# Kernel optimization log

Hardware: AMD Instinct MI355X
Metric: run time of the kernel (lower is better)

Reference implementation:

```python
import jax, jax.numpy as jnp
import numpy as np

BLOCK = 128  # fp8 block-quant block size (128, 128)


def dequant_block_fp8_weight(w, scale_inv):
    """w: [O, I] fp8-valued weights (stored as f32); scale_inv: [O//128, I//128].
    Dequant = per-(128,128)-block multiply by scale."""
    O, I = w.shape
    wb = w.reshape(O // BLOCK, BLOCK, I // BLOCK, BLOCK)
    wb = wb * scale_inv[:, None, :, None]
    return wb.reshape(O, I)


def setup_inputs() -> dict:
    key = jax.random.key(0)
    ks = jax.random.split(key, 7)
    H, F, T = 5120, 1536, 8192  # hidden, moe_intermediate, tokens
    x = jax.random.normal(ks[0], (T, H), dtype=jnp.float32)
    w_gate = jax.random.normal(ks[1], (F, H), dtype=jnp.float32)
    s_gate = jax.random.uniform(ks[2], (F // BLOCK, H // BLOCK), dtype=jnp.float32) * 0.01 + 1e-4
    w_up = jax.random.normal(ks[3], (F, H), dtype=jnp.float32)
    s_up = jax.random.uniform(ks[4], (F // BLOCK, H // BLOCK), dtype=jnp.float32) * 0.01 + 1e-4
    w_down = jax.random.normal(ks[5], (H, F), dtype=jnp.float32)
    s_down = jax.random.uniform(ks[6], (H // BLOCK, F // BLOCK), dtype=jnp.float32) * 0.01 + 1e-4
    return {"x": x, "w_gate": w_gate, "s_gate": s_gate, "w_up": w_up,
            "s_up": s_up, "w_down": w_down, "s_down": s_down}


def reference(x, w_gate, s_gate, w_up, s_up, w_down, s_down):
    # down_proj(silu(gate_proj(x)) * up_proj(x)), each Linear dequantizing
    # block-scaled fp8 weights first (bias=False everywhere).
    wg = dequant_block_fp8_weight(w_gate, s_gate).astype(x.dtype)
    wu = dequant_block_fp8_weight(w_up, s_up).astype(x.dtype)
    wd = dequant_block_fp8_weight(w_down, s_down).astype(x.dtype)
    gate = jnp.einsum('th,fh->tf', x, wg)  # [T, F]
    up = jnp.einsum('th,fh->tf', x, wu)    # [T, F]
    h = jax.nn.silu(gate) * up
    out = jnp.einsum('tf,hf->th', h, wd)   # [T, H]
    return out
```

## Files before the change

kernel.cpp:

```cpp
#include <hip/hip_runtime.h>


typedef __bf16 bf16x8 __attribute__((ext_vector_type(8)));
typedef float  f32x4  __attribute__((ext_vector_type(4)));

#define BK 32

__device__ __forceinline__ void stage128x32(const __bf16* __restrict__ gbase,
                                            __bf16* lds, int ldk, int tid) {
#pragma unroll
  for (int i = 0; i < 2; ++i) {
    int c = tid + i * 256;
    int row = c >> 2;
    int q = c & 3;
    const __bf16* g = gbase + (size_t)row * ldk + q * 8;
    __builtin_amdgcn_global_load_lds(
        (const __attribute__((address_space(1))) void*)g,
        (__attribute__((address_space(3))) void*)(lds + c * 8),
        16, 0, 0);
  }
}

__global__ void xcast(const float* __restrict__ in, __bf16* __restrict__ out,
                      size_t n) {
  size_t idx = ((size_t)blockIdx.x * blockDim.x + threadIdx.x) * 8;
  if (idx >= n) return;
  f32x4 a = *(const f32x4*)(in + idx);
  f32x4 b = *(const f32x4*)(in + idx + 4);
  bf16x8 o;
#pragma unroll
  for (int i = 0; i < 4; ++i) { o[i] = (__bf16)a[i]; o[i + 4] = (__bf16)b[i]; }
  *(bf16x8*)(out + idx) = o;
}

__global__ void dequant8(const float* __restrict__ w,
                         const float* __restrict__ s,
                         __bf16* __restrict__ o, int rows, int cols) {
  size_t idx = ((size_t)blockIdx.x * blockDim.x + threadIdx.x) * 8;
  if (idx >= (size_t)rows * (size_t)cols) return;
  int r = (int)(idx / cols);
  int c = (int)(idx % cols);
  float sc = s[(r >> 7) * (cols >> 7) + (c >> 7)];
  f32x4 a = *(const f32x4*)(w + idx);
  f32x4 b = *(const f32x4*)(w + idx + 4);
  bf16x8 ov;
#pragma unroll
  for (int i = 0; i < 4; ++i) {
    ov[i] = (__bf16)(a[i] * sc);
    ov[i + 4] = (__bf16)(b[i] * sc);
  }
  *(bf16x8*)(o + idx) = ov;
}

__global__ __launch_bounds__(256, 2)
void gateup_gemm(const __bf16* __restrict__ X, const __bf16* __restrict__ Wg,
                 const __bf16* __restrict__ Wu, __bf16* __restrict__ Hout,
                 int M, int N, int K) {
  __shared__ __bf16 sA[128 * BK];
  __shared__ __bf16 sBg[128 * BK];
  __shared__ __bf16 sBu[128 * BK];
  const int tid = threadIdx.x;
  const int lane = tid & 63;
  const int wave = tid >> 6;
  const int wm = (wave >> 1) * 64;
  const int wn = (wave & 1) * 64;
  const int m0 = blockIdx.y * 128;
  const int n0 = blockIdx.x * 128;
  const int lr = lane & 15;
  const int lk = (lane >> 4) * 8;

  f32x4 accg[4][4] = {};
  f32x4 accu[4][4] = {};

  const __bf16* Ab = X + (size_t)m0 * K;
  const __bf16* Gb = Wg + (size_t)n0 * K;
  const __bf16* Ub = Wu + (size_t)n0 * K;

  for (int k0 = 0; k0 < K; k0 += BK) {
    stage128x32(Ab + k0, sA, K, tid);
    stage128x32(Gb + k0, sBg, K, tid);
    stage128x32(Ub + k0, sBu, K, tid);
    __syncthreads();
    bf16x8 af[4];
#pragma unroll
    for (int i = 0; i < 4; ++i)
      af[i] = *(const bf16x8*)(sA + (wm + i * 16 + lr) * BK + lk);
#pragma unroll
    for (int j = 0; j < 4; ++j) {
      bf16x8 bg = *(const bf16x8*)(sBg + (wn + j * 16 + lr) * BK + lk);
      bf16x8 bu = *(const bf16x8*)(sBu + (wn + j * 16 + lr) * BK + lk);
#pragma unroll
      for (int i = 0; i < 4; ++i) {
        accg[i][j] =
            __builtin_amdgcn_mfma_f32_16x16x32_bf16(af[i], bg, accg[i][j], 0, 0, 0);
        accu[i][j] =
            __builtin_amdgcn_mfma_f32_16x16x32_bf16(af[i], bu, accu[i][j], 0, 0, 0);
      }
    }
    __syncthreads();
  }

  const int colb = n0 + wn + lr;
  const int rowb = m0 + wm + (lane >> 4) * 4;
#pragma unroll
  for (int i = 0; i < 4; ++i)
#pragma unroll
    for (int j = 0; j < 4; ++j)
#pragma unroll
      for (int r = 0; r < 4; ++r) {
        float g = accg[i][j][r];
        float u = accu[i][j][r];
        float hv = (g / (1.0f + __expf(-g))) * u;
        Hout[(size_t)(rowb + i * 16 + r) * N + (colb + j * 16)] = (__bf16)hv;
      }
}

__global__ void down_gemm(const __bf16* __restrict__ A,
                          const __bf16* __restrict__ B,
                          float* __restrict__ C, int M, int N, int K) {
  __shared__ __bf16 sA[128 * BK];
  __shared__ __bf16 sB[128 * BK];
  const int tid = threadIdx.x;
  const int lane = tid & 63;
  const int wave = tid >> 6;
  const int wm = (wave >> 1) * 64;
  const int wn = (wave & 1) * 64;
  const int m0 = blockIdx.y * 128;
  const int n0 = blockIdx.x * 128;
  const int lr = lane & 15;
  const int lk = (lane >> 4) * 8;

  f32x4 acc[4][4] = {};

  const __bf16* Ab = A + (size_t)m0 * K;
  const __bf16* Bb = B + (size_t)n0 * K;

  for (int k0 = 0; k0 < K; k0 += BK) {
    stage128x32(Ab + k0, sA, K, tid);
    stage128x32(Bb + k0, sB, K, tid);
    __syncthreads();
    bf16x8 af[4];
#pragma unroll
    for (int i = 0; i < 4; ++i)
      af[i] = *(const bf16x8*)(sA + (wm + i * 16 + lr) * BK + lk);
#pragma unroll
    for (int j = 0; j < 4; ++j) {
      bf16x8 bf = *(const bf16x8*)(sB + (wn + j * 16 + lr) * BK + lk);
#pragma unroll
      for (int i = 0; i < 4; ++i)
        acc[i][j] =
            __builtin_amdgcn_mfma_f32_16x16x32_bf16(af[i], bf, acc[i][j], 0, 0, 0);
    }
    __syncthreads();
  }

  const int colb = n0 + wn + lr;
  const int rowb = m0 + wm + (lane >> 4) * 4;
#pragma unroll
  for (int i = 0; i < 4; ++i)
#pragma unroll
    for (int j = 0; j < 4; ++j)
#pragma unroll
      for (int r = 0; r < 4; ++r)
        C[(size_t)(rowb + i * 16 + r) * N + (colb + j * 16)] = acc[i][j][r];
}

extern "C" void kernel_launch(void* const* d_in, const int* in_sizes, int n_in,
                              void* d_out, int out_size, void* d_ws,
                              size_t ws_size, hipStream_t stream) {
  const int Hd = 5120, Fd = 1536, Td = 8192;
  const float* x = (const float*)d_in[0];
  const float* wg = (const float*)d_in[1];
  const float* sg = (const float*)d_in[2];
  const float* wu = (const float*)d_in[3];
  const float* su = (const float*)d_in[4];
  const float* wd = (const float*)d_in[5];
  const float* sd = (const float*)d_in[6];
  float* out = (float*)d_out;

  __bf16* ws = (__bf16*)d_ws;
  const size_t xsz = (size_t)Td * (size_t)Hd;
  const size_t wsz = (size_t)Fd * (size_t)Hd;
  __bf16* xb = ws;
  __bf16* wgq = xb + xsz;
  __bf16* wuq = wgq + wsz;
  __bf16* wdq = wuq + wsz;
  __bf16* hbuf = wdq + wsz;

  xcast<<<(int)(xsz / 8 / 256), 256, 0, stream>>>(x, xb, xsz);

  const int dq_blocks = (int)(wsz / 8 / 256);
  dequant8<<<dq_blocks, 256, 0, stream>>>(wg, sg, wgq, Fd, Hd);
  dequant8<<<dq_blocks, 256, 0, stream>>>(wu, su, wuq, Fd, Hd);
  dequant8<<<dq_blocks, 256, 0, stream>>>(wd, sd, wdq, Hd, Fd);

  dim3 g1(Fd / 128, Td / 128);
  gateup_gemm<<<g1, 256, 0, stream>>>(xb, wgq, wuq, hbuf, Td, Fd, Hd);

  dim3 g2(Hd / 128, Td / 128);
  down_gemm<<<g2, 256, 0, stream>>>(hbuf, wdq, out, Td, Hd, Fd);
}
```

Baseline: 827.5 us.

## Interleave gate/up weights into one GEMM and merge prep kernels into one launch

```diff
diff --git a/kernel.cpp b/kernel.cpp
--- a/kernel.cpp
+++ b/kernel.cpp
@@ -21,10 +21,8 @@
   }
 }
 
-__global__ void xcast(const float* __restrict__ in, __bf16* __restrict__ out,
-                      size_t n) {
-  size_t idx = ((size_t)blockIdx.x * blockDim.x + threadIdx.x) * 8;
-  if (idx >= n) return;
+__device__ __forceinline__ void cast8(const float* __restrict__ in,
+                                      __bf16* __restrict__ out, size_t idx) {
   f32x4 a = *(const f32x4*)(in + idx);
   f32x4 b = *(const f32x4*)(in + idx + 4);
   bf16x8 o;
@@ -33,91 +31,65 @@
   *(bf16x8*)(out + idx) = o;
 }
 
-__global__ void dequant8(const float* __restrict__ w,
-                         const float* __restrict__ s,
-                         __bf16* __restrict__ o, int rows, int cols) {
-  size_t idx = ((size_t)blockIdx.x * blockDim.x + threadIdx.x) * 8;
-  if (idx >= (size_t)rows * (size_t)cols) return;
-  int r = (int)(idx / cols);
-  int c = (int)(idx % cols);
-  float sc = s[(r >> 7) * (cols >> 7) + (c >> 7)];
+__device__ __forceinline__ void dq_ilv(const float* __restrict__ w,
+                                       const float* __restrict__ s,
+                                       __bf16* __restrict__ wq, int r, int tid,
+                                       int which) {
+  unsigned idx = ((unsigned)r * 256u + (unsigned)tid) * 8u;
+  unsigned f = idx / 5120u;
+  unsigned h = idx - f * 5120u;
+  float sc = s[(f >> 7) * 40 + (h >> 7)];
   f32x4 a = *(const f32x4*)(w + idx);
   f32x4 b = *(const f32x4*)(w + idx + 4);
-  bf16x8 ov;
+  bf16x8 o;
 #pragma unroll
   for (int i = 0; i < 4; ++i) {
-    ov[i] = (__bf16)(a[i] * sc);
-    ov[i + 4] = (__bf16)(b[i] * sc);
+    o[i] = (__bf16)(a[i] * sc);
+    o[i + 4] = (__bf16)(b[i] * sc);
   }
-  *(bf16x8*)(o + idx) = ov;
+  *(bf16x8*)(wq + (size_t)(2 * f + which) * 5120 + h) = o;
 }
 
-__global__ __launch_bounds__(256, 2)
-void gateup_gemm(const __bf16* __restrict__ X, const __bf16* __restrict__ Wg,
-                 const __bf16* __restrict__ Wu, __bf16* __restrict__ Hout,
-                 int M, int N, int K) {
-  __shared__ __bf16 sA[128 * BK];
-  __shared__ __bf16 sBg[128 * BK];
-  __shared__ __bf16 sBu[128 * BK];
-  const int tid = threadIdx.x;
-  const int lane = tid & 63;
-  const int wave = tid >> 6;
-  const int wm = (wave >> 1) * 64;
-  const int wn = (wave & 1) * 64;
-  const int m0 = blockIdx.y * 128;
-  const int n0 = blockIdx.x * 128;
-  const int lr = lane & 15;
-  const int lk = (lane >> 4) * 8;
-
-  f32x4 accg[4][4] = {};
-  f32x4 accu[4][4] = {};
-
-  const __bf16* Ab = X + (size_t)m0 * K;
-  const __bf16* Gb = Wg + (size_t)n0 * K;
-  const __bf16* Ub = Wu + (size_t)n0 * K;
-
-  for (int k0 = 0; k0 < K; k0 += BK) {
-    stage128x32(Ab + k0, sA, K, tid);
-    stage128x32(Gb + k0, sBg, K, tid);
-    stage128x32(Ub + k0, sBu, K, tid);
-    __syncthreads();
-    bf16x8 af[4];
+__device__ __forceinline__ void dq_wd(const float* __restrict__ w,
+                                      const float* __restrict__ s,
+                                      __bf16* __restrict__ o8, int r, int tid) {
+  unsigned idx = ((unsigned)r * 256u + (unsigned)tid) * 8u;
+  unsigned f = idx / 1536u;
+  unsigned h = idx - f * 1536u;
+  float sc = s[(f >> 7) * 12 + (h >> 7)];
+  f32x4 a = *(const f32x4*)(w + idx);
+  f32x4 b = *(const f32x4*)(w + idx + 4);
+  bf16x8 o;
 #pragma unroll
-    for (int i = 0; i < 4; ++i)
-      af[i] = *(const bf16x8*)(sA + (wm + i * 16 + lr) * BK + lk);
-#pragma unroll
-    for (int j = 0; j < 4; ++j) {
-      bf16x8 bg = *(const bf16x8*)(sBg + (wn + j * 16 + lr) * BK + lk);
-      bf16x8 bu = *(const bf16x8*)(sBu + (wn + j * 16 + lr) * BK + lk);
-#pragma unroll
-      for (int i = 0; i < 4; ++i) {
-        accg[i][j] =
-            __builtin_amdgcn_mfma_f32_16x16x32_bf16(af[i], bg, accg[i][j], 0, 0, 0);
-        accu[i][j] =
-            __builtin_amdgcn_mfma_f32_16x16x32_bf16(af[i], bu, accu[i][j], 0, 0, 0);
-      }
-    }
-    __syncthreads();
+  for (int i = 0; i < 4; ++i) {
+    o[i] = (__bf16)(a[i] * sc);
+    o[i + 4] = (__bf16)(b[i] * sc);
   }
-
-  const int colb = n0 + wn + lr;
-  const int rowb = m0 + wm + (lane >> 4) * 4;
-#pragma unroll
-  for (int i = 0; i < 4; ++i)
-#pragma unroll
-    for (int j = 0; j < 4; ++j)
-#pragma unroll
-      for (int r = 0; r < 4; ++r) {
-        float g = accg[i][j][r];
-        float u = accu[i][j][r];
-        float hv = (g / (1.0f + __expf(-g))) * u;
-        Hout[(size_t)(rowb + i * 16 + r) * N + (colb + j * 16)] = (__bf16)hv;
-      }
+  *(bf16x8*)(o8 + idx) = o;
 }
 
-__global__ void down_gemm(const __bf16* __restrict__ A,
-                          const __bf16* __restrict__ B,
-                          float* __restrict__ C, int M, int N, int K) {
+__global__ void prep(const float* __restrict__ x, const float* __restrict__ wg,
+                     const float* __restrict__ sg, const float* __restrict__ wu,
+                     const float* __restrict__ su, const float* __restrict__ wd,
+                     const float* __restrict__ sd, __bf16* __restrict__ xb,
+                     __bf16* __restrict__ wq, __bf16* __restrict__ wdq) {
+  int bid = blockIdx.x;
+  int tid = threadIdx.x;
+  if (bid < 20480) {
+    cast8(x, xb, ((size_t)bid * 256 + tid) * 8);
+  } else if (bid < 24320) {
+    dq_ilv(wg, sg, wq, bid - 20480, tid, 0);
+  } else if (bid < 28160) {
+    dq_ilv(wu, su, wq, bid - 24320, tid, 1);
+  } else {
+    dq_wd(wd, sd, wdq, bid - 28160, tid);
+  }
+}
+
+template <bool FUSE_SILU, typename OutT>
+__global__ void gemm_bt(const __bf16* __restrict__ A,
+                        const __bf16* __restrict__ B, OutT* __restrict__ C,
+                        int M, int N, int K, int ldc) {
   __shared__ __bf16 sA[128 * BK];
   __shared__ __bf16 sB[128 * BK];
   const int tid = threadIdx.x;
@@ -161,8 +133,21 @@
 #pragma unroll
     for (int j = 0; j < 4; ++j)
 #pragma unroll
-      for (int r = 0; r < 4; ++r)
-        C[(size_t)(rowb + i * 16 + r) * N + (colb + j * 16)] = acc[i][j][r];
+      for (int r = 0; r < 4; ++r) {
+        if constexpr (FUSE_SILU) {
+          float v = acc[i][j][r];
+          float p = __shfl_xor(v, 1, 64);
+          float g = (lane & 1) ? p : v;
+          float u = (lane & 1) ? v : p;
+          float hv = (g / (1.0f + __expf(-g))) * u;
+          if ((lane & 1) == 0)
+            C[(size_t)(rowb + i * 16 + r) * ldc + ((colb + j * 16) >> 1)] =
+                (OutT)hv;
+        } else {
+          C[(size_t)(rowb + i * 16 + r) * ldc + (colb + j * 16)] =
+              (OutT)acc[i][j][r];
+        }
+      }
 }
 
 extern "C" void kernel_launch(void* const* d_in, const int* in_sizes, int n_in,
@@ -179,24 +164,18 @@
   float* out = (float*)d_out;
 
   __bf16* ws = (__bf16*)d_ws;
-  const size_t xsz = (size_t)Td * (size_t)Hd;
-  const size_t wsz = (size_t)Fd * (size_t)Hd;
+  const size_t xsz = (size_t)Td * Hd;
   __bf16* xb = ws;
-  __bf16* wgq = xb + xsz;
-  __bf16* wuq = wgq + wsz;
-  __bf16* wdq = wuq + wsz;
-  __bf16* hbuf = wdq + wsz;
+  __bf16* wq = xb + xsz;
+  __bf16* wdq = wq + (size_t)2 * Fd * Hd;
+  __bf16* hbuf = wdq + (size_t)Hd * Fd;
 
-  xcast<<<(int)(xsz / 8 / 256), 256, 0, stream>>>(x, xb, xsz);
+  prep<<<32000, 256, 0, stream>>>(x, wg, sg, wu, su, wd, sd, xb, wq, wdq);
 
-  const int dq_blocks = (int)(wsz / 8 / 256);
-  dequant8<<<dq_blocks, 256, 0, stream>>>(wg, sg, wgq, Fd, Hd);
-  dequant8<<<dq_blocks, 256, 0, stream>>>(wu, su, wuq, Fd, Hd);
-  dequant8<<<dq_blocks, 256, 0, stream>>>(wd, sd, wdq, Hd, Fd);
-
-  dim3 g1(Fd / 128, Td / 128);
-  gateup_gemm<<<g1, 256, 0, stream>>>(xb, wgq, wuq, hbuf, Td, Fd, Hd);
+  dim3 g1(2 * Fd / 128, Td / 128);
+  gemm_bt<true, __bf16><<<g1, 256, 0, stream>>>(xb, wq, hbuf, Td, 2 * Fd, Hd,
+                                                Fd);
 
   dim3 g2(Hd / 128, Td / 128);
-  down_gemm<<<g2, 256, 0, stream>>>(hbuf, wdq, out, Td, Hd, Fd);
+  gemm_bt<false, float><<<g2, 256, 0, stream>>>(hbuf, wdq, out, Td, Hd, Fd, Hd);
 }
```

New measurement: 810.0 us. 1.02x faster.
